# Kernel optimization log

Measured on AMD Instinct MI355X. Metric: run time of the kernel, lower is better.

The kernel has to match this reference:

```python
import jax, jax.numpy as jnp
import numpy as np

VF = 3          # vote_factor
GRID = 0.1      # grid_size
P = 4           # padded per-group capacity (stands in for data-dependent max group size)
RATIO_MAX = 5   # original drops groups needing repeat ratio > 5
EPS = 1e-5
SHIFT, BASE = 512, 1024  # 3D->1D hash (int32-safe: BASE**3 < 2**31)


def _bn_relu(x, gamma, beta):
    # BatchNorm1d in train mode over the token (batch) axis; conv input is (N, C, 1)
    m = x.mean(axis=0)
    v = jnp.mean((x - m) ** 2, axis=0)  # biased variance, as torch BN uses for normalization
    return jax.nn.relu((x - m) * jax.lax.rsqrt(v + EPS) * gamma + beta)


def _one_sample(idv, cov, ftv, W1, b1, g1, be1, W2, b2, g2, be2, W3, b3):
    N, C = ftv.shape
    V = N * VF
    # conv1x1 stack == per-token linear layers
    h = _bn_relu(ftv @ W1.T + b1, g1, be1)
    h = _bn_relu(h @ W2.T + b2, g2, be2)
    log = (h @ W3.T + b3).reshape(N, VF, 3 + C)
    off3 = log[:, :, :3]                                  # (N, VF, 3)
    coor = (cov[:, None, :] + off3).reshape(V, 3)
    grid_res = (off3 / GRID).astype(jnp.int32)            # trunc toward zero, like .int()
    ind = (idv[:, None, :] + grid_res).reshape(V, 3)
    # Degenerate inner-dict loop (tensor keys hash by identity): every vote's feature
    # offset becomes offset[n][VF-1] * 3 / VF  (len(key)==3, idx stale at VF-1)
    feat_off = log[:, VF - 1, 3:] * (3.0 / VF)            # (N, C)
    feat = jnp.broadcast_to((ftv + feat_off)[:, None, :], (N, VF, C)).reshape(V, C)

    # group votes by quantized 3D index (tuple-key dict -> hash + unique + segment ops)
    hc = jnp.clip(ind, -SHIFT, SHIFT - 1) + SHIFT
    keys = (hc[:, 0] * BASE + hc[:, 1]) * BASE + hc[:, 2]  # (V,) int32
    _, inv = jnp.unique(keys, size=V, fill_value=-1, return_inverse=True)
    inv = inv.reshape(-1)
    ones = jnp.ones((V,), jnp.int32)
    counts = jax.ops.segment_sum(ones, inv, num_segments=V)          # group sizes
    order = jnp.argsort(inv)                                          # votes sorted by group
    starts = jnp.cumsum(counts) - counts
    first = jax.ops.segment_min(jnp.arange(V, dtype=jnp.int32), inv, num_segments=V)
    first = jnp.where(counts > 0, first, 0)
    ind_buf = jnp.where((counts > 0)[:, None], ind[first], 0).astype(jnp.int32)

    cnt_safe = jnp.maximum(counts, 1)
    p = jnp.arange(P, dtype=jnp.int32)
    src_pos = starts[:, None] + (p[None, :] % cnt_safe[:, None])      # (V, P) repeat-fill
    src = order[src_pos]
    valid = (counts > 0) & (counts * RATIO_MAX >= P)                  # ceil(P/cnt) <= 5
    coor_buf = jnp.where(valid[:, None, None], coor[src], 0.0)        # (V, P, 3)
    feat_buf = jnp.where(valid[:, None, None], feat[src], 0.0)        # (V, P, C)
    return ind_buf, coor_buf, feat_buf, valid


def setup_inputs() -> dict:
    key = jax.random.key(0)
    ks = jax.random.split(key, 12)
    B, N, C = 2, 16384, 128
    s = 1.0 / np.sqrt(C)
    return {
        "ID": jax.random.randint(ks[0], (B, N, 3), 0, 100, dtype=jnp.int32),
        "CO": jax.random.normal(ks[1], (B, N, 3), jnp.float32),
        "FT": jax.random.normal(ks[2], (B, N, C), jnp.float32),
        "W1": jax.random.normal(ks[3], (C, C), jnp.float32) * s,
        "b1": jnp.zeros((C,), jnp.float32),
        "g1": 1.0 + 0.1 * jax.random.normal(ks[4], (C,), jnp.float32),
        "be1": 0.1 * jax.random.normal(ks[5], (C,), jnp.float32),
        "W2": jax.random.normal(ks[6], (C, C), jnp.float32) * s,
        "b2": jnp.zeros((C,), jnp.float32),
        "g2": 1.0 + 0.1 * jax.random.normal(ks[7], (C,), jnp.float32),
        "be2": 0.1 * jax.random.normal(ks[8], (C,), jnp.float32),
        "W3": jax.random.normal(ks[9], ((3 + C) * VF, C), jnp.float32) * s,
        "b3": 0.01 * jax.random.normal(ks[10], ((3 + C) * VF,), jnp.float32),
    }


def reference(ID, CO, FT, W1, b1, g1, be1, W2, b2, g2, be2, W3, b3):
    outs = [_one_sample(ID[i], CO[i], FT[i], W1, b1, g1, be1, W2, b2, g2, be2, W3, b3)
            for i in range(ID.shape[0])]  # small fixed batch loop
    ind_buf = jnp.stack([o[0] for o in outs])
    coor_buf = jnp.stack([o[1] for o in outs])
    feat_buf = jnp.stack([o[2] for o in outs])
    mask = jnp.stack([o[3] for o in outs])
    return ind_buf, coor_buf, feat_buf, mask
```

## Files before the change

kernel.cpp:

```cpp
#include <hip/hip_runtime.h>

constexpr int Bn = 2;
constexpr int Nn = 16384;
constexpr int Cc = 128;
constexpr int Vv = Nn * 3;
constexpr int Pp = 4;
constexpr int SB = 48;
constexpr int HB = 96;

constexpr size_t IND0  = 0;
constexpr size_t COOR0 = (size_t)Bn * Vv * 3;
constexpr size_t FEAT0 = COOR0 + (size_t)Bn * Vv * Pp * 3;
constexpr size_t MASK0 = FEAT0 + (size_t)Bn * Vv * Pp * Cc;

template<bool BN>
__global__ __launch_bounds__(256) void gemm_t(
    const float* __restrict__ A, const float* __restrict__ W,
    const float* __restrict__ bias, const float* __restrict__ ss,
    float* __restrict__ out)
{
    __shared__ float As[64 * 36];
    __shared__ float Ws[128 * 36];

    int bid = blockIdx.x;
    int s = bid >> 8, rb = bid & 255;
    const float* Ag = A + (size_t)s * Nn * Cc + (size_t)rb * 64 * Cc;
    float* outg = out + (size_t)s * Nn * Cc + (size_t)rb * 64 * Cc;
    const float* sp = nullptr;
    if constexpr (BN) sp = ss + (size_t)s * 2 * Cc;

    int t = threadIdx.x, tx = t & 15, ty = t >> 4;

    float acc[4][8];
    #pragma unroll
    for (int i = 0; i < 4; ++i)
        #pragma unroll
        for (int j = 0; j < 8; ++j) acc[i][j] = 0.f;

    for (int stage = 0; stage < 4; ++stage) {
        int k0 = stage * 32;
        if (stage) __syncthreads();
        #pragma unroll
        for (int r = 0; r < 2; ++r) {
            int idx = r * 256 + t;
            int row = idx >> 3, c4 = (idx & 7) * 4;
            float4 v = *(const float4*)(Ag + (size_t)row * Cc + k0 + c4);
            if constexpr (BN) {
                int ch = k0 + c4;
                v.x = fmaxf(0.f, fmaf(v.x, sp[ch + 0], sp[Cc + ch + 0]));
                v.y = fmaxf(0.f, fmaf(v.y, sp[ch + 1], sp[Cc + ch + 1]));
                v.z = fmaxf(0.f, fmaf(v.z, sp[ch + 2], sp[Cc + ch + 2]));
                v.w = fmaxf(0.f, fmaf(v.w, sp[ch + 3], sp[Cc + ch + 3]));
            }
            *(float4*)&As[row * 36 + c4] = v;
        }
        #pragma unroll
        for (int r = 0; r < 4; ++r) {
            int idx = r * 256 + t;
            int row = idx >> 3, c4 = (idx & 7) * 4;
            *(float4*)&Ws[row * 36 + c4] = *(const float4*)(W + (size_t)row * Cc + k0 + c4);
        }
        __syncthreads();
        #pragma unroll
        for (int k4 = 0; k4 < 8; ++k4) {
            int k = k4 * 4;
            float4 av[4];
            #pragma unroll
            for (int i = 0; i < 4; ++i) av[i] = *(const float4*)&As[(i * 16 + ty) * 36 + k];
            #pragma unroll
            for (int j = 0; j < 8; ++j) {
                float4 wv = *(const float4*)&Ws[(j * 16 + tx) * 36 + k];
                #pragma unroll
                for (int i = 0; i < 4; ++i) {
                    float a0 = acc[i][j];
                    a0 = fmaf(av[i].x, wv.x, a0);
                    a0 = fmaf(av[i].y, wv.y, a0);
                    a0 = fmaf(av[i].z, wv.z, a0);
                    a0 = fmaf(av[i].w, wv.w, a0);
                    acc[i][j] = a0;
                }
            }
        }
    }
    #pragma unroll
    for (int j = 0; j < 8; ++j) {
        int col = j * 16 + tx;
        float bv = bias[col];
        #pragma unroll
        for (int i = 0; i < 4; ++i)
            outg[(size_t)(i * 16 + ty) * Cc + col] = acc[i][j] + bv;
    }
}

__global__ __launch_bounds__(256) void gemm3_fused(
    const float* __restrict__ A, const float* __restrict__ W,
    const float* __restrict__ bias, const float* __restrict__ ss,
    const float* __restrict__ FT, const float* __restrict__ CO,
    const int* __restrict__ ID,
    float* __restrict__ featb, float* __restrict__ coor,
    int* __restrict__ indb, unsigned* __restrict__ keys,
    unsigned* __restrict__ idx0, unsigned* __restrict__ hist0)
{
    __shared__ float As[64 * 36];
    __shared__ float Ws[144 * 36];

    int bid = blockIdx.x;
    int s = bid >> 8, rb = bid & 255;
    const float* Ag = A + (size_t)s * Nn * Cc + (size_t)rb * 64 * Cc;
    const float* sp = ss + (size_t)s * 2 * Cc;

    int t = threadIdx.x, tx = t & 15, ty = t >> 4;

    float acc[4][9];
    #pragma unroll
    for (int i = 0; i < 4; ++i)
        #pragma unroll
        for (int j = 0; j < 9; ++j) acc[i][j] = 0.f;

    for (int stage = 0; stage < 4; ++stage) {
        int k0 = stage * 32;
        if (stage) __syncthreads();
        #pragma unroll
        for (int r = 0; r < 2; ++r) {
            int idx = r * 256 + t;
            int row = idx >> 3, c4 = (idx & 7) * 4;
            float4 v = *(const float4*)(Ag + (size_t)row * Cc + k0 + c4);
            int ch = k0 + c4;
            v.x = fmaxf(0.f, fmaf(v.x, sp[ch + 0], sp[Cc + ch + 0]));
            v.y = fmaxf(0.f, fmaf(v.y, sp[ch + 1], sp[Cc + ch + 1]));
            v.z = fmaxf(0.f, fmaf(v.z, sp[ch + 2], sp[Cc + ch + 2]));
            v.w = fmaxf(0.f, fmaf(v.w, sp[ch + 3], sp[Cc + ch + 3]));
            *(float4*)&As[row * 36 + c4] = v;
        }
        for (int idx = t; idx < 144 * 8; idx += 256) {
            int row = idx >> 3, c4 = (idx & 7) * 4;
            float4 v = make_float4(0.f, 0.f, 0.f, 0.f);
            if (row < 137) {
                int wr = (row < 9) ? (row / 3) * 131 + (row % 3) : row + 256;
                v = *(const float4*)(W + (size_t)wr * Cc + k0 + c4);
            }
            *(float4*)&Ws[row * 36 + c4] = v;
        }
        __syncthreads();
        #pragma unroll
        for (int k4 = 0; k4 < 8; ++k4) {
            int k = k4 * 4;
            float4 av[4];
            #pragma unroll
            for (int i = 0; i < 4; ++i) av[i] = *(const float4*)&As[(i * 16 + ty) * 36 + k];
            #pragma unroll
            for (int j = 0; j < 9; ++j) {
                float4 wv = *(const float4*)&Ws[(j * 16 + tx) * 36 + k];
                #pragma unroll
                for (int i = 0; i < 4; ++i) {
                    float a0 = acc[i][j];
                    a0 = fmaf(av[i].x, wv.x, a0);
                    a0 = fmaf(av[i].y, wv.y, a0);
                    a0 = fmaf(av[i].z, wv.z, a0);
                    a0 = fmaf(av[i].w, wv.w, a0);
                    acc[i][j] = a0;
                }
            }
        }
    }

    __syncthreads();
    __shared__ float L9[64 * 12];
    int n0 = rb * 64;
    const float* FTg = FT + ((size_t)s * Nn + n0) * Cc;
    float* FBg = featb + ((size_t)s * Nn + n0) * Cc;
    #pragma unroll
    for (int j = 0; j < 9; ++j) {
        int col = j * 16 + tx;
        if (col < 9) {
            float bv = bias[(col / 3) * 131 + col % 3];
            #pragma unroll
            for (int i = 0; i < 4; ++i)
                L9[(i * 16 + ty) * 12 + col] = acc[i][j] + bv;
        } else if (col < 137) {
            int ch = col - 9;
            float bv = bias[col + 256];
            #pragma unroll
            for (int i = 0; i < 4; ++i) {
                int row = i * 16 + ty;
                float lg = acc[i][j] + bv;
                FBg[(size_t)row * Cc + ch] = FTg[(size_t)row * Cc + ch] + lg;
            }
        }
    }
    __syncthreads();
    if (t < 192) {
        int row = t / 3, jv = t - row * 3;
        int n = n0 + row, v = n * 3 + jv;
        size_t vb = (size_t)s * Vv + v;
        float o0 = L9[row * 12 + jv * 3 + 0];
        float o1 = L9[row * 12 + jv * 3 + 1];
        float o2 = L9[row * 12 + jv * 3 + 2];
        const float* co = CO + ((size_t)s * Nn + n) * 3;
        coor[vb * 3 + 0] = co[0] + o0;
        coor[vb * 3 + 1] = co[1] + o1;
        coor[vb * 3 + 2] = co[2] + o2;
        const int* id = ID + ((size_t)s * Nn + n) * 3;
        int gi0 = (int)(o0 / 0.1f), gi1 = (int)(o1 / 0.1f), gi2 = (int)(o2 / 0.1f);
        int i0 = id[0] + gi0, i1 = id[1] + gi1, i2 = id[2] + gi2;
        indb[vb * 3 + 0] = i0; indb[vb * 3 + 1] = i1; indb[vb * 3 + 2] = i2;
        int h0 = min(max(i0, -512), 511) + 512;
        int h1 = min(max(i1, -512), 511) + 512;
        int h2 = min(max(i2, -512), 511) + 512;
        unsigned key = ((unsigned)h0 * 1024u + (unsigned)h1) * 1024u + (unsigned)h2;
        keys[vb] = key;
        idx0[vb] = (unsigned)v;
        atomicAdd(&hist0[(size_t)s * SB * 1024 + (size_t)(v >> 10) * 1024 + (key & 1023u)], 1u);
    }
}

__global__ void colstats(const float* __restrict__ Y, float* __restrict__ part)
{
    int blk = blockIdx.x;
    int s = blk >> 6, b = blk & 63;
    const float* Yp = Y + (size_t)s * Nn * Cc + (size_t)b * 256 * Cc;
    int c = threadIdx.x;
    float sm = 0.f, sq = 0.f;
    for (int r = 0; r < 256; ++r) {
        float v = Yp[(size_t)r * Cc + c];
        sm += v; sq += v * v;
    }
    float* pp = part + ((size_t)s * 64 + b) * 2 * Cc;
    pp[c] = sm;
    pp[Cc + c] = sq;
}

__global__ void bnfinalize(const float* __restrict__ part, const float* __restrict__ g,
                           const float* __restrict__ be, float* __restrict__ ss)
{
    int s = blockIdx.x, c = threadIdx.x;
    const float* pp = part + (size_t)s * 64 * 2 * Cc;
    float sm = 0.f, sq = 0.f;
    for (int b = 0; b < 64; ++b) {
        sm += pp[(size_t)b * 2 * Cc + c];
        sq += pp[(size_t)b * 2 * Cc + Cc + c];
    }
    float m   = sm / (float)Nn;
    float var = sq / (float)Nn - m * m;
    float inv = 1.0f / sqrtf(var + 1e-5f);
    float sc  = g[c] * inv;
    ss[(size_t)s * 2 * Cc + c]      = sc;
    ss[(size_t)s * 2 * Cc + Cc + c] = be[c] - m * sc;
}

__global__ void zerok(uint4* __restrict__ p)
{
    p[(size_t)blockIdx.x * 256 + threadIdx.x] = make_uint4(0, 0, 0, 0);
}

template<int PASS>
__global__ __launch_bounds__(512) void scat(
    const unsigned* __restrict__ kIn, const unsigned* __restrict__ iIn,
    unsigned* __restrict__ kOut, unsigned* __restrict__ iOut,
    const unsigned* __restrict__ hist, unsigned* __restrict__ nextH)
{
    __shared__ unsigned hw[8 * 1024];
    __shared__ unsigned tot[1024];
    int t = threadIdx.x, lane = t & 63, w = t >> 6;
    int blk = blockIdx.x, s = blk / SB, b = blk % SB;

    #pragma unroll
    for (int i = 0; i < 16; ++i) hw[w * 1024 + i * 64 + lane] = 0u;

    const uint2* hs2 = (const uint2*)(hist + (size_t)s * SB * 1024);
    int d0 = 2 * t, d1 = 2 * t + 1;
    unsigned run0 = 0, run1 = 0, my0 = 0, my1 = 0;
    for (int bb = 0; bb < SB; ++bb) {
        uint2 v = hs2[bb * 512 + t];
        if (bb == b) { my0 = run0; my1 = run1; }
        run0 += v.x; run1 += v.y;
    }
    tot[d0] = run0; tot[d1] = run1;
    __syncthreads();
    for (int ofs = 1; ofs < 1024; ofs <<= 1) {
        unsigned a0 = (d0 >= ofs) ? tot[d0 - ofs] : 0u;
        unsigned a1 = (d1 >= ofs) ? tot[d1 - ofs] : 0u;
        __syncthreads();
        tot[d0] += a0; tot[d1] += a1;
        __syncthreads();
    }
    tot[d0] = tot[d0] - run0 + my0;
    tot[d1] = tot[d1] - run1 + my1;

    size_t base = (size_t)s * Vv + (size_t)b * 1024;
    unsigned keyE[2], idxE[2], rkE[2], dE[2];
    #pragma unroll
    for (int e = 0; e < 2; ++e) {
        int pos = w * 128 + e * 64 + lane;
        keyE[e] = kIn[base + pos];
        idxE[e] = iIn[base + pos];
        unsigned d = (keyE[e] >> (PASS * 10)) & 1023u;
        dE[e] = d;
        unsigned long long m = ~0ull;
        #pragma unroll
        for (int bit = 0; bit < 10; ++bit) {
            bool bbit = (d >> bit) & 1u;
            unsigned long long bal = __ballot(bbit);
            m &= bbit ? bal : ~bal;
        }
        int lanesBelow = __popcll(m & ((1ull << lane) - 1ull));
        int cnt = __popcll(m);
        int leader = __ffsll((unsigned long long)m) - 1;
        unsigned basec = hw[w * 1024 + d];
        if (lane == leader) hw[w * 1024 + d] = basec + (unsigned)cnt;
        rkE[e] = basec + (unsigned)lanesBelow;
    }
    __syncthreads();
    {
        unsigned r0 = 0, r1 = 0;
        for (int ww = 0; ww < 8; ++ww) {
            unsigned v0 = hw[ww * 1024 + d0], v1 = hw[ww * 1024 + d1];
            hw[ww * 1024 + d0] = r0; hw[ww * 1024 + d1] = r1;
            r0 += v0; r1 += v1;
        }
    }
    __syncthreads();
    #pragma unroll
    for (int e = 0; e < 2; ++e) {
        unsigned dest = tot[dE[e]] + hw[w * 1024 + dE[e]] + rkE[e];
        kOut[(size_t)s * Vv + dest] = keyE[e];
        iOut[(size_t)s * Vv + dest] = idxE[e];
        if constexpr (PASS < 2) {
            unsigned d2 = (keyE[e] >> ((PASS + 1) * 10)) & 1023u;
            atomicAdd(&nextH[(size_t)s * SB * 1024 + (size_t)(dest >> 10) * 1024 + d2], 1u);
        }
    }
}

__global__ __launch_bounds__(512) void headsct(const unsigned* __restrict__ skeys,
                                               unsigned* __restrict__ hpart)
{
    int blk = blockIdx.x;
    int s = blk / HB, b = blk % HB;
    int i = b * 512 + threadIdx.x;
    size_t base = (size_t)s * Vv;
    unsigned k = skeys[base + i];
    bool head = (i == 0) || (skeys[base + i - 1] != k);
    __shared__ unsigned wsum[8];
    unsigned long long bal = __ballot(head);
    int lane = threadIdx.x & 63, wid = threadIdx.x >> 6;
    if (lane == 0) wsum[wid] = (unsigned)__popcll(bal);
    __syncthreads();
    if (threadIdx.x == 0) {
        unsigned tot = 0;
        for (int w = 0; w < 8; ++w) tot += wsum[w];
        hpart[s * HB + b] = tot;
    }
}

__global__ __launch_bounds__(512) void ranksk(const unsigned* __restrict__ skeys,
                                              const unsigned* __restrict__ hpart,
                                              unsigned* __restrict__ start,
                                              unsigned* __restrict__ nu)
{
    int blk = blockIdx.x;
    int s = blk / HB, b = blk % HB;
    int t = threadIdx.x;
    __shared__ unsigned hp[HB];
    __shared__ unsigned pre[HB + 1];
    if (t < HB) hp[t] = hpart[s * HB + t];
    __syncthreads();
    if (t == 0) {
        unsigned run = 0;
        for (int i = 0; i < HB; ++i) { pre[i] = run; run += hp[i]; }
        pre[HB] = run;
    }
    __syncthreads();
    int i = b * 512 + t;
    size_t base = (size_t)s * Vv;
    unsigned k = skeys[base + i];
    bool head = (i == 0) || (skeys[base + i - 1] != k);
    unsigned long long bal = __ballot(head);
    int lane = t & 63, wid = t >> 6;
    __shared__ unsigned wsum[8];
    if (lane == 0) wsum[wid] = (unsigned)__popcll(bal);
    __syncthreads();
    unsigned wbase = 0;
    for (int w = 0; w < wid; ++w) wbase += wsum[w];
    unsigned lpre = (unsigned)__popcll(bal & ((1ull << lane) - 1ull));
    if (head)
        start[(size_t)s * (Vv + 1) + pre[b] + wbase + lpre] = (unsigned)i;
    if (b == 0 && t == 0) {
        nu[s] = pre[HB];
        start[(size_t)s * (Vv + 1) + pre[HB]] = (unsigned)Vv;
    }
}

__global__ __launch_bounds__(256) void outputk(
    const unsigned* __restrict__ sidx, const unsigned* __restrict__ start,
    const unsigned* __restrict__ nu, const int* __restrict__ indb,
    const float* __restrict__ coor, const float* __restrict__ featb,
    float* __restrict__ out)
{
    int wid = threadIdx.x >> 6, lane = threadIdx.x & 63;
    int g = blockIdx.x * 4 + wid;
    int s = g / Vv, u = g - s * Vv;
    size_t su = (size_t)s * Vv + u;
    bool valid = (unsigned)u < nu[s];
    float4* out4 = (float4*)out;
    int f = lane & 31, jlo = lane >> 5;
    if (valid) {
        const unsigned* st = start + (size_t)s * (Vv + 1);
        unsigned i0 = st[u], i1 = st[u + 1];
        unsigned c = i1 - i0;
        unsigned my = sidx[(size_t)s * Vv + i0 + ((unsigned)(lane & 3)) % c];
        unsigned sv[4];
        sv[0] = __shfl(my, 0); sv[1] = __shfl(my, 1);
        sv[2] = __shfl(my, 2); sv[3] = __shfl(my, 3);
        const float4* fb = (const float4*)(featb + (size_t)s * Nn * Cc);
        #pragma unroll
        for (int h = 0; h < 2; ++h) {
            int j = jlo + 2 * h;
            out4[(FEAT0 >> 2) + su * 128 + (size_t)j * 32 + f] =
                fb[(size_t)(sv[j] / 3) * 32 + f];
        }
        if (lane < 12)
            out[COOR0 + su * 12 + lane] =
                coor[((size_t)s * Vv + sv[lane / 3]) * 3 + lane % 3];
        else if (lane < 15)
            out[IND0 + su * 3 + (lane - 12)] =
                (float)indb[((size_t)s * Vv + sv[0]) * 3 + (lane - 12)];
        else if (lane == 15)
            out[MASK0 + su] = 1.f;
    } else {
        float4 z = make_float4(0.f, 0.f, 0.f, 0.f);
        #pragma unroll
        for (int h = 0; h < 2; ++h)
            out4[(FEAT0 >> 2) + su * 128 + (size_t)(jlo + 2 * h) * 32 + f] = z;
        if (lane < 12)       out[COOR0 + su * 12 + lane] = 0.f;
        else if (lane < 15)  out[IND0 + su * 3 + (lane - 12)] = 0.f;
        else if (lane == 15) out[MASK0 + su] = 0.f;
    }
}

extern "C" void kernel_launch(void* const* d_in, const int* in_sizes, int n_in,
                              void* d_out, int out_size, void* d_ws, size_t ws_size,
                              hipStream_t stream)
{
    const int*   ID  = (const int*)d_in[0];
    const float* CO  = (const float*)d_in[1];
    const float* FT  = (const float*)d_in[2];
    const float* W1  = (const float*)d_in[3];
    const float* b1  = (const float*)d_in[4];
    const float* g1  = (const float*)d_in[5];
    const float* be1 = (const float*)d_in[6];
    const float* W2  = (const float*)d_in[7];
    const float* b2  = (const float*)d_in[8];
    const float* g2  = (const float*)d_in[9];
    const float* be2 = (const float*)d_in[10];
    const float* W3  = (const float*)d_in[11];
    const float* b3  = (const float*)d_in[12];
    float* out = (float*)d_out;

    char* wsc = (char*)d_ws;
    size_t off = 0;
    auto alloc = [&](size_t elems) -> void* {
        void* p = wsc + off;
        off += ((elems * 4 + 255) & ~(size_t)255);
        return p;
    };
    float*    H1b   = (float*)alloc((size_t)Bn * Nn * Cc);
    float*    H2b   = (float*)alloc((size_t)Bn * Nn * Cc);
    float*    PART  = (float*)alloc((size_t)Bn * 64 * 2 * Cc);
    float*    SS    = (float*)alloc((size_t)Bn * 2 * Cc);
    float*    COORb = (float*)alloc((size_t)Bn * Vv * 3);
    int*      INDB  = (int*)alloc((size_t)Bn * Vv * 3);
    float*    FEATB = (float*)alloc((size_t)Bn * Nn * Cc);
    unsigned* KA    = (unsigned*)alloc((size_t)Bn * Vv);
    unsigned* IA    = (unsigned*)alloc((size_t)Bn * Vv);
    unsigned* KB    = (unsigned*)alloc((size_t)Bn * Vv);
    unsigned* IB    = (unsigned*)alloc((size_t)Bn * Vv);
    unsigned* H0h   = (unsigned*)alloc((size_t)Bn * SB * 1024);
    unsigned* H1h   = (unsigned*)alloc((size_t)Bn * SB * 1024);
    unsigned* H2h   = (unsigned*)alloc((size_t)Bn * SB * 1024);
    unsigned* HP    = (unsigned*)alloc((size_t)Bn * HB);
    unsigned* NUp   = (unsigned*)alloc((size_t)Bn);
    unsigned* STp   = (unsigned*)alloc((size_t)Bn * (Vv + 1));
    (void)in_sizes; (void)n_in; (void)out_size; (void)ws_size;

    zerok<<<288, 256, 0, stream>>>((uint4*)H0h);

    gemm_t<false><<<Bn * 256, 256, 0, stream>>>(FT, W1, b1, nullptr, H1b);
    colstats<<<Bn * 64, 128, 0, stream>>>(H1b, PART);
    bnfinalize<<<Bn, 128, 0, stream>>>(PART, g1, be1, SS);
    gemm_t<true><<<Bn * 256, 256, 0, stream>>>(H1b, W2, b2, SS, H2b);
    colstats<<<Bn * 64, 128, 0, stream>>>(H2b, PART);
    bnfinalize<<<Bn, 128, 0, stream>>>(PART, g2, be2, SS);

    gemm3_fused<<<Bn * 256, 256, 0, stream>>>(H2b, W3, b3, SS, FT, CO, ID,
                                              FEATB, COORb, INDB, KA, IA, H0h);

    scat<0><<<Bn * SB, 512, 0, stream>>>(KA, IA, KB, IB, H0h, H1h);
    scat<1><<<Bn * SB, 512, 0, stream>>>(KB, IB, KA, IA, H1h, H2h);
    scat<2><<<Bn * SB, 512, 0, stream>>>(KA, IA, KB, IB, H2h, nullptr);

    headsct<<<Bn * HB, 512, 0, stream>>>(KB, HP);
    ranksk<<<Bn * HB, 512, 0, stream>>>(KB, HP, STp, NUp);

    outputk<<<Bn * Vv / 4, 256, 0, stream>>>(IB, STp, NUp, INDB, COORb, FEATB, out);
}
```

Measured before the change: 213.3 us.

## Merge radix sort and ranking into one persistent kernel with grid barriers

Replaces the three scatter launches plus the head-count and rank kernels with a single persistent kernel of 96 blocks that uses atomic-counter grid barriers between phases. BN finalize is folded into the stats kernel through a last-block-done counter, and histogram zeroing is folded into the first GEMM. Output feature stores become nontemporal. The aim is to cut kernel launch count and launch gaps. The cost is spin-wait barriers whose progress depends on all 96 blocks being co-resident.

Result: slower. 235.8 us (+10.6%).

```diff
diff --git a/kernel.cpp b/kernel.cpp
--- a/kernel.cpp
+++ b/kernel.cpp
@@ -1,4 +1,6 @@
 #include <hip/hip_runtime.h>
+
+typedef float f4 __attribute__((ext_vector_type(4)));
 
 constexpr int Bn = 2;
 constexpr int Nn = 16384;
@@ -6,21 +8,29 @@
 constexpr int Vv = Nn * 3;
 constexpr int Pp = 4;
 constexpr int SB = 48;
-constexpr int HB = 96;
+constexpr int NBLK = Bn * SB;
 
 constexpr size_t IND0  = 0;
 constexpr size_t COOR0 = (size_t)Bn * Vv * 3;
 constexpr size_t FEAT0 = COOR0 + (size_t)Bn * Vv * Pp * 3;
 constexpr size_t MASK0 = FEAT0 + (size_t)Bn * Vv * Pp * Cc;
 
-template<bool BN>
+template<bool BN, bool ZERO>
 __global__ __launch_bounds__(256) void gemm_t(
     const float* __restrict__ A, const float* __restrict__ W,
     const float* __restrict__ bias, const float* __restrict__ ss,
-    float* __restrict__ out)
+    float* __restrict__ out, unsigned* __restrict__ HZ, unsigned* __restrict__ CNT)
 {
     __shared__ float As[64 * 36];
     __shared__ float Ws[128 * 36];
+
+    int t = threadIdx.x;
+    if constexpr (ZERO) {
+        int gid = blockIdx.x * 256 + t;
+        if (gid < 3 * Bn * SB * 1024 / 4)
+            ((uint4*)HZ)[gid] = make_uint4(0u, 0u, 0u, 0u);
+        if (gid < 8) CNT[gid] = 0u;
+    }
 
     int bid = blockIdx.x;
     int s = bid >> 8, rb = bid & 255;
@@ -29,7 +39,7 @@
     const float* sp = nullptr;
     if constexpr (BN) sp = ss + (size_t)s * 2 * Cc;
 
-    int t = threadIdx.x, tx = t & 15, ty = t >> 4;
+    int tx = t & 15, ty = t >> 4;
 
     float acc[4][8];
     #pragma unroll
@@ -214,7 +224,9 @@
     }
 }
 
-__global__ void colstats(const float* __restrict__ Y, float* __restrict__ part)
+__global__ void statsbnf(const float* __restrict__ Y, float* __restrict__ part,
+                         const float* __restrict__ g, const float* __restrict__ be,
+                         float* __restrict__ ss, unsigned* __restrict__ cnt)
 {
     int blk = blockIdx.x;
     int s = blk >> 6, b = blk & 63;
@@ -228,41 +240,60 @@
     float* pp = part + ((size_t)s * 64 + b) * 2 * Cc;
     pp[c] = sm;
     pp[Cc + c] = sq;
-}
-
-__global__ void bnfinalize(const float* __restrict__ part, const float* __restrict__ g,
-                           const float* __restrict__ be, float* __restrict__ ss)
-{
-    int s = blockIdx.x, c = threadIdx.x;
-    const float* pp = part + (size_t)s * 64 * 2 * Cc;
-    float sm = 0.f, sq = 0.f;
-    for (int b = 0; b < 64; ++b) {
-        sm += pp[(size_t)b * 2 * Cc + c];
-        sq += pp[(size_t)b * 2 * Cc + Cc + c];
-    }
-    float m   = sm / (float)Nn;
-    float var = sq / (float)Nn - m * m;
-    float inv = 1.0f / sqrtf(var + 1e-5f);
-    float sc  = g[c] * inv;
-    ss[(size_t)s * 2 * Cc + c]      = sc;
-    ss[(size_t)s * 2 * Cc + Cc + c] = be[c] - m * sc;
-}
-
-__global__ void zerok(uint4* __restrict__ p)
-{
-    p[(size_t)blockIdx.x * 256 + threadIdx.x] = make_uint4(0, 0, 0, 0);
-}
+
+    __shared__ unsigned flag;
+    __syncthreads();
+    if (threadIdx.x == 0) {
+        __threadfence();
+        unsigned old = atomicAdd(cnt, 1u);
+        flag = (old == 127u) ? 1u : 0u;
+    }
+    __syncthreads();
+    if (flag) {
+        __threadfence();
+        for (int s2 = 0; s2 < Bn; ++s2) {
+            const float* pq = part + (size_t)s2 * 64 * 2 * Cc;
+            float s1 = 0.f, s2q = 0.f;
+            for (int b2 = 0; b2 < 64; ++b2) {
+                s1  += pq[(size_t)b2 * 2 * Cc + c];
+                s2q += pq[(size_t)b2 * 2 * Cc + Cc + c];
+            }
+            float m   = s1 / (float)Nn;
+            float var = s2q / (float)Nn - m * m;
+            float inv = 1.0f / sqrtf(var + 1e-5f);
+            float sc  = g[c] * inv;
+            ss[(size_t)s2 * 2 * Cc + c]      = sc;
+            ss[(size_t)s2 * 2 * Cc + Cc + c] = be[c] - m * sc;
+        }
+    }
+}
+
+__device__ __forceinline__ void gbar(unsigned* bar)
+{
+    __syncthreads();
+    if (threadIdx.x == 0) {
+        __threadfence();
+        atomicAdd(bar, 1u);
+        while (__hip_atomic_load(bar, __ATOMIC_RELAXED, __HIP_MEMORY_SCOPE_AGENT)
+               < (unsigned)NBLK)
+            __builtin_amdgcn_s_sleep(4);
+        __threadfence();
+    }
+    __syncthreads();
+}
+
+struct SortArgs {
+    unsigned *KA, *IA, *KB, *IB, *H0, *H1, *H2, *HP, *NU, *ST, *BAR;
+};
 
 template<int PASS>
-__global__ __launch_bounds__(512) void scat(
-    const unsigned* __restrict__ kIn, const unsigned* __restrict__ iIn,
-    unsigned* __restrict__ kOut, unsigned* __restrict__ iOut,
-    const unsigned* __restrict__ hist, unsigned* __restrict__ nextH)
-{
-    __shared__ unsigned hw[8 * 1024];
-    __shared__ unsigned tot[1024];
-    int t = threadIdx.x, lane = t & 63, w = t >> 6;
-    int blk = blockIdx.x, s = blk / SB, b = blk % SB;
+__device__ void scat_phase(int bid, int t, unsigned* hw, unsigned* tot,
+                           const unsigned* kIn, const unsigned* iIn,
+                           unsigned* kOut, unsigned* iOut,
+                           const unsigned* hist, unsigned* nextH)
+{
+    int lane = t & 63, w = t >> 6;
+    int s = bid / SB, b = bid % SB;
 
     #pragma unroll
     for (int i = 0; i < 16; ++i) hw[w * 1024 + i * 64 + lane] = 0u;
@@ -332,63 +363,64 @@
     }
 }
 
-__global__ __launch_bounds__(512) void headsct(const unsigned* __restrict__ skeys,
-                                               unsigned* __restrict__ hpart)
-{
-    int blk = blockIdx.x;
-    int s = blk / HB, b = blk % HB;
-    int i = b * 512 + threadIdx.x;
+__global__ __launch_bounds__(512) void sortall(SortArgs a)
+{
+    __shared__ unsigned hw[8 * 1024];
+    __shared__ unsigned tot[1024];
+    int t = threadIdx.x, bid = blockIdx.x;
+
+    scat_phase<0>(bid, t, hw, tot, a.KA, a.IA, a.KB, a.IB, a.H0, a.H1);
+    gbar(a.BAR + 0);
+    scat_phase<1>(bid, t, hw, tot, a.KB, a.IB, a.KA, a.IA, a.H1, a.H2);
+    gbar(a.BAR + 1);
+    scat_phase<2>(bid, t, hw, tot, a.KA, a.IA, a.KB, a.IB, a.H2, nullptr);
+    gbar(a.BAR + 2);
+
+    int s = bid / SB, cb = bid % SB;
+    int lane = t & 63, w = t >> 6;
     size_t base = (size_t)s * Vv;
-    unsigned k = skeys[base + i];
-    bool head = (i == 0) || (skeys[base + i - 1] != k);
-    __shared__ unsigned wsum[8];
-    unsigned long long bal = __ballot(head);
-    int lane = threadIdx.x & 63, wid = threadIdx.x >> 6;
-    if (lane == 0) wsum[wid] = (unsigned)__popcll(bal);
-    __syncthreads();
-    if (threadIdx.x == 0) {
-        unsigned tot = 0;
-        for (int w = 0; w < 8; ++w) tot += wsum[w];
-        hpart[s * HB + b] = tot;
-    }
-}
-
-__global__ __launch_bounds__(512) void ranksk(const unsigned* __restrict__ skeys,
-                                              const unsigned* __restrict__ hpart,
-                                              unsigned* __restrict__ start,
-                                              unsigned* __restrict__ nu)
-{
-    int blk = blockIdx.x;
-    int s = blk / HB, b = blk % HB;
-    int t = threadIdx.x;
-    __shared__ unsigned hp[HB];
-    __shared__ unsigned pre[HB + 1];
-    if (t < HB) hp[t] = hpart[s * HB + t];
-    __syncthreads();
+    int p0 = cb * 1024 + t;
+    int p1 = p0 + 512;
+    unsigned k0 = a.KB[base + p0];
+    unsigned k1 = a.KB[base + p1];
+    bool h0 = (p0 == 0) || (a.KB[base + p0 - 1] != k0);
+    bool h1 = (a.KB[base + p1 - 1] != k1);
+    unsigned long long bal0 = __ballot(h0);
+    unsigned long long bal1 = __ballot(h1);
+    if (lane == 0) {
+        tot[w]     = (unsigned)__popcll(bal0);
+        tot[8 + w] = (unsigned)__popcll(bal1);
+    }
+    __syncthreads();
+    if (t == 0) {
+        unsigned sum = 0;
+        for (int i = 0; i < 16; ++i) sum += tot[i];
+        a.HP[bid] = sum;
+    }
+    gbar(a.BAR + 3);
+
     if (t == 0) {
         unsigned run = 0;
-        for (int i = 0; i < HB; ++i) { pre[i] = run; run += hp[i]; }
-        pre[HB] = run;
-    }
-    __syncthreads();
-    int i = b * 512 + t;
-    size_t base = (size_t)s * Vv;
-    unsigned k = skeys[base + i];
-    bool head = (i == 0) || (skeys[base + i - 1] != k);
-    unsigned long long bal = __ballot(head);
-    int lane = t & 63, wid = t >> 6;
-    __shared__ unsigned wsum[8];
-    if (lane == 0) wsum[wid] = (unsigned)__popcll(bal);
-    __syncthreads();
-    unsigned wbase = 0;
-    for (int w = 0; w < wid; ++w) wbase += wsum[w];
-    unsigned lpre = (unsigned)__popcll(bal & ((1ull << lane) - 1ull));
-    if (head)
-        start[(size_t)s * (Vv + 1) + pre[b] + wbase + lpre] = (unsigned)i;
-    if (b == 0 && t == 0) {
-        nu[s] = pre[HB];
-        start[(size_t)s * (Vv + 1) + pre[HB]] = (unsigned)Vv;
-    }
+        for (int i = 0; i < SB; ++i) { tot[32 + i] = run; run += a.HP[s * SB + i]; }
+        if (cb == 0) {
+            a.NU[s] = run;
+            a.ST[(size_t)s * (Vv + 1) + run] = (unsigned)Vv;
+        }
+    }
+    __syncthreads();
+    unsigned mybase = tot[32 + cb];
+    unsigned wbase0 = 0, tot0 = 0, wbase1 = 0;
+    for (int ww = 0; ww < 8; ++ww) {
+        if (ww < w) wbase0 += tot[ww];
+        tot0 += tot[ww];
+        if (ww < w) wbase1 += tot[8 + ww];
+    }
+    wbase1 += tot0;
+    unsigned long long below = (1ull << lane) - 1ull;
+    if (h0)
+        a.ST[(size_t)s * (Vv + 1) + mybase + wbase0 + (unsigned)__popcll(bal0 & below)] = (unsigned)p0;
+    if (h1)
+        a.ST[(size_t)s * (Vv + 1) + mybase + wbase1 + (unsigned)__popcll(bal1 & below)] = (unsigned)p1;
 }
 
 __global__ __launch_bounds__(256) void outputk(
@@ -402,7 +434,7 @@
     int s = g / Vv, u = g - s * Vv;
     size_t su = (size_t)s * Vv + u;
     bool valid = (unsigned)u < nu[s];
-    float4* out4 = (float4*)out;
+    f4* out4 = (f4*)out;
     int f = lane & 31, jlo = lane >> 5;
     if (valid) {
         const unsigned* st = start + (size_t)s * (Vv + 1);
@@ -412,12 +444,12 @@
         unsigned sv[4];
         sv[0] = __shfl(my, 0); sv[1] = __shfl(my, 1);
         sv[2] = __shfl(my, 2); sv[3] = __shfl(my, 3);
-        const float4* fb = (const float4*)(featb + (size_t)s * Nn * Cc);
+        const f4* fb = (const f4*)(featb + (size_t)s * Nn * Cc);
         #pragma unroll
         for (int h = 0; h < 2; ++h) {
             int j = jlo + 2 * h;
-            out4[(FEAT0 >> 2) + su * 128 + (size_t)j * 32 + f] =
-                fb[(size_t)(sv[j] / 3) * 32 + f];
+            __builtin_nontemporal_store(fb[(size_t)(sv[j] / 3) * 32 + f],
+                &out4[(FEAT0 >> 2) + su * 128 + (size_t)j * 32 + f]);
         }
         if (lane < 12)
             out[COOR0 + su * 12 + lane] =
@@ -428,10 +460,11 @@
         else if (lane == 15)
             out[MASK0 + su] = 1.f;
     } else {
-        float4 z = make_float4(0.f, 0.f, 0.f, 0.f);
+        f4 z = (f4){0.f, 0.f, 0.f, 0.f};
         #pragma unroll
         for (int h = 0; h < 2; ++h)
-            out4[(FEAT0 >> 2) + su * 128 + (size_t)(jlo + 2 * h) * 32 + f] = z;
+            __builtin_nontemporal_store(z,
+                &out4[(FEAT0 >> 2) + su * 128 + (size_t)(jlo + 2 * h) * 32 + f]);
         if (lane < 12)       out[COOR0 + su * 12 + lane] = 0.f;
         else if (lane < 15)  out[IND0 + su * 3 + (lane - 12)] = 0.f;
         else if (lane == 15) out[MASK0 + su] = 0.f;
@@ -478,29 +511,22 @@
     unsigned* H0h   = (unsigned*)alloc((size_t)Bn * SB * 1024);
     unsigned* H1h   = (unsigned*)alloc((size_t)Bn * SB * 1024);
     unsigned* H2h   = (unsigned*)alloc((size_t)Bn * SB * 1024);
-    unsigned* HP    = (unsigned*)alloc((size_t)Bn * HB);
+    unsigned* HP    = (unsigned*)alloc((size_t)Bn * SB);
     unsigned* NUp   = (unsigned*)alloc((size_t)Bn);
     unsigned* STp   = (unsigned*)alloc((size_t)Bn * (Vv + 1));
+    unsigned* CNT   = (unsigned*)alloc(8);
     (void)in_sizes; (void)n_in; (void)out_size; (void)ws_size;
 
-    zerok<<<288, 256, 0, stream>>>((uint4*)H0h);
-
-    gemm_t<false><<<Bn * 256, 256, 0, stream>>>(FT, W1, b1, nullptr, H1b);
-    colstats<<<Bn * 64, 128, 0, stream>>>(H1b, PART);
-    bnfinalize<<<Bn, 128, 0, stream>>>(PART, g1, be1, SS);
-    gemm_t<true><<<Bn * 256, 256, 0, stream>>>(H1b, W2, b2, SS, H2b);
-    colstats<<<Bn * 64, 128, 0, stream>>>(H2b, PART);
-    bnfinalize<<<Bn, 128, 0, stream>>>(PART, g2, be2, SS);
-
+    gemm_t<false, true><<<Bn * 256, 256, 0, stream>>>(FT, W1, b1, nullptr, H1b, H0h, CNT);
+    statsbnf<<<Bn * 64, 128, 0, stream>>>(H1b, PART, g1, be1, SS, CNT + 0);
+    gemm_t<true, false><<<Bn * 256, 256, 0, stream>>>(H1b, W2, b2, SS, H2b, nullptr, nullptr);
+    statsbnf<<<Bn * 64, 128, 0, stream>>>(H2b, PART, g2, be2, SS, CNT + 1);
     gemm3_fused<<<Bn * 256, 256, 0, stream>>>(H2b, W3, b3, SS, FT, CO, ID,
                                               FEATB, COORb, INDB, KA, IA, H0h);
-
-    scat<0><<<Bn * SB, 512, 0, stream>>>(KA, IA, KB, IB, H0h, H1h);
-    scat<1><<<Bn * SB, 512, 0, stream>>>(KB, IB, KA, IA, H1h, H2h);
-    scat<2><<<Bn * SB, 512, 0, stream>>>(KA, IA, KB, IB, H2h, nullptr);
-
-    headsct<<<Bn * HB, 512, 0, stream>>>(KB, HP);
-    ranksk<<<Bn * HB, 512, 0, stream>>>(KB, HP, STp, NUp);
-
+    SortArgs sa;
+    sa.KA = KA; sa.IA = IA; sa.KB = KB; sa.IB = IB;
+    sa.H0 = H0h; sa.H1 = H1h; sa.H2 = H2h;
+    sa.HP = HP; sa.NU = NUp; sa.ST = STp; sa.BAR = CNT + 2;
+    sortall<<<NBLK, 512, 0, stream>>>(sa);
     outputk<<<Bn * Vv / 4, 256, 0, stream>>>(IB, STp, NUp, INDB, COORb, FEATB, out);
 }
```

## Fuse BN finalize and histogram zeroing into GEMMs, add register prefetch

Applied to the files above, without the earlier changes.

Removes the separate bnfinalize and zerok launches by computing BN scale/shift per block into shared memory inside the following GEMM, and zeroing the histogram buffers inside the first GEMM. The GEMM loops now prefetch the next K-slice of A and W into registers while the current slice is in shared memory. This cuts kernel launches and dependency gaps, at the cost of each block redundantly reducing the 64 partial statistics and using more registers.

After: 214.2 us. Within noise of the previous version (+0.5%).

```diff
diff --git a/kernel.cpp b/kernel.cpp
--- a/kernel.cpp
+++ b/kernel.cpp
@@ -13,23 +13,50 @@
 constexpr size_t FEAT0 = COOR0 + (size_t)Bn * Vv * Pp * 3;
 constexpr size_t MASK0 = FEAT0 + (size_t)Bn * Vv * Pp * Cc;
 
-template<bool BN>
+template<bool BNF, bool ZERO>
 __global__ __launch_bounds__(256) void gemm_t(
     const float* __restrict__ A, const float* __restrict__ W,
-    const float* __restrict__ bias, const float* __restrict__ ss,
-    float* __restrict__ out)
+    const float* __restrict__ bias, const float* __restrict__ part,
+    const float* __restrict__ g, const float* __restrict__ be,
+    float* __restrict__ out, unsigned* __restrict__ HZ)
 {
     __shared__ float As[64 * 36];
     __shared__ float Ws[128 * 36];
+    __shared__ float ssl[2 * Cc];
+
+    int t = threadIdx.x;
+    if constexpr (ZERO) {
+        int gid = blockIdx.x * 256 + t;
+        if (gid < 3 * Bn * SB * 1024 / 4)
+            ((uint4*)HZ)[gid] = make_uint4(0u, 0u, 0u, 0u);
+    }
 
     int bid = blockIdx.x;
     int s = bid >> 8, rb = bid & 255;
     const float* Ag = A + (size_t)s * Nn * Cc + (size_t)rb * 64 * Cc;
     float* outg = out + (size_t)s * Nn * Cc + (size_t)rb * 64 * Cc;
-    const float* sp = nullptr;
-    if constexpr (BN) sp = ss + (size_t)s * 2 * Cc;
-
-    int t = threadIdx.x, tx = t & 15, ty = t >> 4;
+
+    if constexpr (BNF) {
+        if (t < Cc) {
+            const float* pp = part + (size_t)s * 64 * 2 * Cc;
+            float sm = 0.f, sq = 0.f;
+            for (int b = 0; b < 64; ++b) {
+                sm += pp[(size_t)b * 2 * Cc + t];
+                sq += pp[(size_t)b * 2 * Cc + Cc + t];
+            }
+            float m   = sm / (float)Nn;
+            float var = sq / (float)Nn - m * m;
+            float inv = 1.0f / sqrtf(var + 1e-5f);
+            float sc  = g[t] * inv;
+            ssl[t]      = sc;
+            ssl[Cc + t] = be[t] - m * sc;
+        }
+        __syncthreads();
+    }
+
+    int tx = t & 15, ty = t >> 4;
+    int arow = t >> 3, ac4 = (t & 7) * 4;
+    int wrow0 = t >> 3;
 
     float acc[4][8];
     #pragma unroll
@@ -37,28 +64,39 @@
         #pragma unroll
         for (int j = 0; j < 8; ++j) acc[i][j] = 0.f;
 
+    float4 aR[2], wR[4];
+    #pragma unroll
+    for (int r = 0; r < 2; ++r)
+        aR[r] = *(const float4*)(Ag + (size_t)(arow + r * 32) * Cc + ac4);
+    #pragma unroll
+    for (int r = 0; r < 4; ++r)
+        wR[r] = *(const float4*)(W + (size_t)(wrow0 + r * 32) * Cc + ac4);
+
     for (int stage = 0; stage < 4; ++stage) {
-        int k0 = stage * 32;
         if (stage) __syncthreads();
         #pragma unroll
         for (int r = 0; r < 2; ++r) {
-            int idx = r * 256 + t;
-            int row = idx >> 3, c4 = (idx & 7) * 4;
-            float4 v = *(const float4*)(Ag + (size_t)row * Cc + k0 + c4);
-            if constexpr (BN) {
-                int ch = k0 + c4;
-                v.x = fmaxf(0.f, fmaf(v.x, sp[ch + 0], sp[Cc + ch + 0]));
-                v.y = fmaxf(0.f, fmaf(v.y, sp[ch + 1], sp[Cc + ch + 1]));
-                v.z = fmaxf(0.f, fmaf(v.z, sp[ch + 2], sp[Cc + ch + 2]));
-                v.w = fmaxf(0.f, fmaf(v.w, sp[ch + 3], sp[Cc + ch + 3]));
+            float4 v = aR[r];
+            if constexpr (BNF) {
+                int ch = ac4;
+                v.x = fmaxf(0.f, fmaf(v.x, ssl[ch + 0], ssl[Cc + ch + 0]));
+                v.y = fmaxf(0.f, fmaf(v.y, ssl[ch + 1], ssl[Cc + ch + 1]));
+                v.z = fmaxf(0.f, fmaf(v.z, ssl[ch + 2], ssl[Cc + ch + 2]));
+                v.w = fmaxf(0.f, fmaf(v.w, ssl[ch + 3], ssl[Cc + ch + 3]));
             }
-            *(float4*)&As[row * 36 + c4] = v;
-        }
-        #pragma unroll
-        for (int r = 0; r < 4; ++r) {
-            int idx = r * 256 + t;
-            int row = idx >> 3, c4 = (idx & 7) * 4;
-            *(float4*)&Ws[row * 36 + c4] = *(const float4*)(W + (size_t)row * Cc + k0 + c4);
+            *(float4*)&As[(arow + r * 32) * 36 + ac4] = v;
+        }
+        #pragma unroll
+        for (int r = 0; r < 4; ++r)
+            *(float4*)&Ws[(wrow0 + r * 32) * 36 + ac4] = wR[r];
+        if (stage < 3) {
+            int k1 = (stage + 1) * 32;
+            #pragma unroll
+            for (int r = 0; r < 2; ++r)
+                aR[r] = *(const float4*)(Ag + (size_t)(arow + r * 32) * Cc + k1 + ac4);
+            #pragma unroll
+            for (int r = 0; r < 4; ++r)
+                wR[r] = *(const float4*)(W + (size_t)(wrow0 + r * 32) * Cc + k1 + ac4);
         }
         __syncthreads();
         #pragma unroll
@@ -82,6 +120,7 @@
             }
         }
     }
+
     #pragma unroll
     for (int j = 0; j < 8; ++j) {
         int col = j * 16 + tx;
@@ -92,9 +131,124 @@
     }
 }
 
+
+template<bool ZERO>
+__global__ __launch_bounds__(256) void gemm_t2(
+    const float* __restrict__ A, const float* __restrict__ W,
+    const float* __restrict__ bias, const float* __restrict__ part,
+    const float* __restrict__ g, const float* __restrict__ be,
+    float* __restrict__ out, unsigned* __restrict__ HZ)
+{
+    __shared__ float As[64 * 36];
+    __shared__ float Ws[128 * 36];
+    __shared__ float ssl[2 * Cc];
+
+    int t = threadIdx.x;
+    if constexpr (ZERO) {
+        int gid = blockIdx.x * 256 + t;
+        if (gid < 3 * Bn * SB * 1024 / 4)
+            ((uint4*)HZ)[gid] = make_uint4(0u, 0u, 0u, 0u);
+    }
+
+    int bid = blockIdx.x;
+    int s = bid >> 8, rb = bid & 255;
+    const float* Ag = A + (size_t)s * Nn * Cc + (size_t)rb * 64 * Cc;
+    float* outg = out + (size_t)s * Nn * Cc + (size_t)rb * 64 * Cc;
+
+    if (t < Cc) {
+        const float* pp = part + (size_t)s * 64 * 2 * Cc;
+        float sm = 0.f, sq = 0.f;
+        for (int b = 0; b < 64; ++b) {
+            sm += pp[(size_t)b * 2 * Cc + t];
+            sq += pp[(size_t)b * 2 * Cc + Cc + t];
+        }
+        float m   = sm / (float)Nn;
+        float var = sq / (float)Nn - m * m;
+        float inv = 1.0f / sqrtf(var + 1e-5f);
+        float sc  = g[t] * inv;
+        ssl[t]      = sc;
+        ssl[Cc + t] = be[t] - m * sc;
+    }
+    __syncthreads();
+
+    int tx = t & 15, ty = t >> 4;
+    int arow = t >> 3, ac4 = (t & 7) * 4;
+
+    float acc[4][8];
+    #pragma unroll
+    for (int i = 0; i < 4; ++i)
+        #pragma unroll
+        for (int j = 0; j < 8; ++j) acc[i][j] = 0.f;
+
+    float4 aR[2], wR[4];
+    #pragma unroll
+    for (int r = 0; r < 2; ++r)
+        aR[r] = *(const float4*)(Ag + (size_t)(arow + r * 32) * Cc + ac4);
+    #pragma unroll
+    for (int r = 0; r < 4; ++r)
+        wR[r] = *(const float4*)(W + (size_t)(arow + r * 32) * Cc + ac4);
+
+    for (int stage = 0; stage < 4; ++stage) {
+        int k0 = stage * 32;
+        if (stage) __syncthreads();
+        #pragma unroll
+        for (int r = 0; r < 2; ++r) {
+            float4 v = aR[r];
+            int ch = k0 + ac4;
+            v.x = fmaxf(0.f, fmaf(v.x, ssl[ch + 0], ssl[Cc + ch + 0]));
+            v.y = fmaxf(0.f, fmaf(v.y, ssl[ch + 1], ssl[Cc + ch + 1]));
+            v.z = fmaxf(0.f, fmaf(v.z, ssl[ch + 2], ssl[Cc + ch + 2]));
+            v.w = fmaxf(0.f, fmaf(v.w, ssl[ch + 3], ssl[Cc + ch + 3]));
+            *(float4*)&As[(arow + r * 32) * 36 + ac4] = v;
+        }
+        #pragma unroll
+        for (int r = 0; r < 4; ++r)
+            *(float4*)&Ws[(arow + r * 32) * 36 + ac4] = wR[r];
+        if (stage < 3) {
+            int k1 = k0 + 32;
+            #pragma unroll
+            for (int r = 0; r < 2; ++r)
+                aR[r] = *(const float4*)(Ag + (size_t)(arow + r * 32) * Cc + k1 + ac4);
+            #pragma unroll
+            for (int r = 0; r < 4; ++r)
+                wR[r] = *(const float4*)(W + (size_t)(arow + r * 32) * Cc + k1 + ac4);
+        }
+        __syncthreads();
+        #pragma unroll
+        for (int k4 = 0; k4 < 8; ++k4) {
+            int k = k4 * 4;
+            float4 av[4];
+            #pragma unroll
+            for (int i = 0; i < 4; ++i) av[i] = *(const float4*)&As[(i * 16 + ty) * 36 + k];
+            #pragma unroll
+            for (int j = 0; j < 8; ++j) {
+                float4 wv = *(const float4*)&Ws[(j * 16 + tx) * 36 + k];
+                #pragma unroll
+                for (int i = 0; i < 4; ++i) {
+                    float a0 = acc[i][j];
+                    a0 = fmaf(av[i].x, wv.x, a0);
+                    a0 = fmaf(av[i].y, wv.y, a0);
+                    a0 = fmaf(av[i].z, wv.z, a0);
+                    a0 = fmaf(av[i].w, wv.w, a0);
+                    acc[i][j] = a0;
+                }
+            }
+        }
+    }
+    #pragma unroll
+    for (int j = 0; j < 8; ++j) {
+        int col = j * 16 + tx;
+        float bv = bias[col];
+        #pragma unroll
+        for (int i = 0; i < 4; ++i)
+            outg[(size_t)(i * 16 + ty) * Cc + col] = acc[i][j] + bv;
+    }
+}
+
 __global__ __launch_bounds__(256) void gemm3_fused(
     const float* __restrict__ A, const float* __restrict__ W,
-    const float* __restrict__ bias, const float* __restrict__ ss,
+    const float* __restrict__ bias, const float* __restrict__ part,
+    const float* __restrict__ g, const float* __restrict__ be,
     const float* __restrict__ FT, const float* __restrict__ CO,
     const int* __restrict__ ID,
     float* __restrict__ featb, float* __restrict__ coor,
@@ -103,13 +257,29 @@
 {
     __shared__ float As[64 * 36];
     __shared__ float Ws[144 * 36];
+    __shared__ float ssl[2 * Cc];
 
     int bid = blockIdx.x;
     int s = bid >> 8, rb = bid & 255;
     const float* Ag = A + (size_t)s * Nn * Cc + (size_t)rb * 64 * Cc;
-    const float* sp = ss + (size_t)s * 2 * Cc;
 
     int t = threadIdx.x, tx = t & 15, ty = t >> 4;
+
+    if (t < Cc) {
+        const float* pp = part + (size_t)s * 64 * 2 * Cc;
+        float sm = 0.f, sq = 0.f;
+        for (int b = 0; b < 64; ++b) {
+            sm += pp[(size_t)b * 2 * Cc + t];
+            sq += pp[(size_t)b * 2 * Cc + Cc + t];
+        }
+        float m   = sm / (float)Nn;
+        float var = sq / (float)Nn - m * m;
+        float inv = 1.0f / sqrtf(var + 1e-5f);
+        float sc  = g[t] * inv;
+        ssl[t]      = sc;
+        ssl[Cc + t] = be[t] - m * sc;
+    }
+    __syncthreads();
 
     float acc[4][9];
     #pragma unroll
@@ -126,10 +296,10 @@
             int row = idx >> 3, c4 = (idx & 7) * 4;
             float4 v = *(const float4*)(Ag + (size_t)row * Cc + k0 + c4);
             int ch = k0 + c4;
-            v.x = fmaxf(0.f, fmaf(v.x, sp[ch + 0], sp[Cc + ch + 0]));
-            v.y = fmaxf(0.f, fmaf(v.y, sp[ch + 1], sp[Cc + ch + 1]));
-            v.z = fmaxf(0.f, fmaf(v.z, sp[ch + 2], sp[Cc + ch + 2]));
-            v.w = fmaxf(0.f, fmaf(v.w, sp[ch + 3], sp[Cc + ch + 3]));
+            v.x = fmaxf(0.f, fmaf(v.x, ssl[ch + 0], ssl[Cc + ch + 0]));
+            v.y = fmaxf(0.f, fmaf(v.y, ssl[ch + 1], ssl[Cc + ch + 1]));
+            v.z = fmaxf(0.f, fmaf(v.z, ssl[ch + 2], ssl[Cc + ch + 2]));
+            v.w = fmaxf(0.f, fmaf(v.w, ssl[ch + 3], ssl[Cc + ch + 3]));
             *(float4*)&As[row * 36 + c4] = v;
         }
         for (int idx = t; idx < 144 * 8; idx += 256) {
@@ -230,29 +400,6 @@
     pp[Cc + c] = sq;
 }
 
-__global__ void bnfinalize(const float* __restrict__ part, const float* __restrict__ g,
-                           const float* __restrict__ be, float* __restrict__ ss)
-{
-    int s = blockIdx.x, c = threadIdx.x;
-    const float* pp = part + (size_t)s * 64 * 2 * Cc;
-    float sm = 0.f, sq = 0.f;
-    for (int b = 0; b < 64; ++b) {
-        sm += pp[(size_t)b * 2 * Cc + c];
-        sq += pp[(size_t)b * 2 * Cc + Cc + c];
-    }
-    float m   = sm / (float)Nn;
-    float var = sq / (float)Nn - m * m;
-    float inv = 1.0f / sqrtf(var + 1e-5f);
-    float sc  = g[c] * inv;
-    ss[(size_t)s * 2 * Cc + c]      = sc;
-    ss[(size_t)s * 2 * Cc + Cc + c] = be[c] - m * sc;
-}
-
-__global__ void zerok(uint4* __restrict__ p)
-{
-    p[(size_t)blockIdx.x * 256 + threadIdx.x] = make_uint4(0, 0, 0, 0);
-}
-
 template<int PASS>
 __global__ __launch_bounds__(512) void scat(
     const unsigned* __restrict__ kIn, const unsigned* __restrict__ iIn,
@@ -467,7 +614,6 @@
     float*    H1b   = (float*)alloc((size_t)Bn * Nn * Cc);
     float*    H2b   = (float*)alloc((size_t)Bn * Nn * Cc);
     float*    PART  = (float*)alloc((size_t)Bn * 64 * 2 * Cc);
-    float*    SS    = (float*)alloc((size_t)Bn * 2 * Cc);
     float*    COORb = (float*)alloc((size_t)Bn * Vv * 3);
     int*      INDB  = (int*)alloc((size_t)Bn * Vv * 3);
     float*    FEATB = (float*)alloc((size_t)Bn * Nn * Cc);
@@ -483,24 +629,18 @@
     unsigned* STp   = (unsigned*)alloc((size_t)Bn * (Vv + 1));
     (void)in_sizes; (void)n_in; (void)out_size; (void)ws_size;
 
-    zerok<<<288, 256, 0, stream>>>((uint4*)H0h);
-
-    gemm_t<false><<<Bn * 256, 256, 0, stream>>>(FT, W1, b1, nullptr, H1b);
+    gemm_t<false, true><<<Bn * 256, 256, 0, stream>>>(
+        FT, W1, b1, nullptr, nullptr, nullptr, H1b, H0h);
     colstats<<<Bn * 64, 128, 0, stream>>>(H1b, PART);
-    bnfinalize<<<Bn, 128, 0, stream>>>(PART, g1, be1, SS);
-    gemm_t<true><<<Bn * 256, 256, 0, stream>>>(H1b, W2, b2, SS, H2b);
+    gemm_t2<false><<<Bn * 256, 256, 0, stream>>>(
+        H1b, W2, b2, PART, g1, be1, H2b, nullptr);
     colstats<<<Bn * 64, 128, 0, stream>>>(H2b, PART);
-    bnfinalize<<<Bn, 128, 0, stream>>>(PART, g2, be2, SS);
-
-    gemm3_fused<<<Bn * 256, 256, 0, stream>>>(H2b, W3, b3, SS, FT, CO, ID,
-                                              FEATB, COORb, INDB, KA, IA, H0h);
-
+    gemm3_fused<<<Bn * 256, 256, 0, stream>>>(
+        H2b, W3, b3, PART, g2, be2, FT, CO, ID, FEATB, COORb, INDB, KA, IA, H0h);
     scat<0><<<Bn * SB, 512, 0, stream>>>(KA, IA, KB, IB, H0h, H1h);
     scat<1><<<Bn * SB, 512, 0, stream>>>(KB, IB, KA, IA, H1h, H2h);
     scat<2><<<Bn * SB, 512, 0, stream>>>(KA, IA, KB, IB, H2h, nullptr);
-
     headsct<<<Bn * HB, 512, 0, stream>>>(KB, HP);
     ranksk<<<Bn * HB, 512, 0, stream>>>(KB, HP, STp, NUp);
-
     outputk<<<Bn * Vv / 4, 256, 0, stream>>>(IB, STp, NUp, INDB, COORb, FEATB, out);
 }
```
